# Performance work log

Hardware: AMD Instinct MI355X
Metric: run time of the kernel (lower is better)

Reference implementation:

```python
import jax, jax.numpy as jnp
import numpy as np

EPS = 1e-6
H = 8          # num_heads
GAMMA = 0.99   # fixed decay (requires_grad=False in source)
RPE_LAYERS = 3


def srms(x):
    # SimpleRMSNorm: x / (rms(x) + eps), rms = ||x||_2 / sqrt(d) = sqrt(mean(x^2))
    return x / (jnp.sqrt(jnp.mean(x * x, axis=-1, keepdims=True)) + EPS)


def setup_inputs() -> dict:
    key = jax.random.key(0)
    B, N, E = 8, 2048, 512
    D1 = 1536            # int(3*512) // 8 * 8
    R = 512              # rpe_embedding
    ks = jax.random.split(key, 12)

    def lin(k, i, o):
        return jax.random.normal(k, (i, o), jnp.float32) * (i ** -0.5)

    x = jax.random.normal(ks[0], (B, N, E), jnp.float32)
    return {
        "x": x,
        "Wu": lin(ks[1], E, D1), "bu": jnp.zeros((D1,), jnp.float32),
        "Wv": lin(ks[2], E, D1), "bv": jnp.zeros((D1,), jnp.float32),
        "Wo": lin(ks[3], D1, E), "bo": jnp.zeros((E,), jnp.float32),
        "rpe_Win": lin(ks[4], 1, R), "rpe_bin": jnp.zeros((R,), jnp.float32),
        "rpe_W": jax.random.normal(ks[5], (RPE_LAYERS, R, R), jnp.float32) * (R ** -0.5),
        "rpe_b": jnp.zeros((RPE_LAYERS, R), jnp.float32),
        "rpe_Wout": lin(ks[6], R, D1), "rpe_bout": jnp.zeros((D1,), jnp.float32),
    }


def reference(x, Wu, bu, Wv, bv, Wo, bo, rpe_Win, rpe_bin, rpe_W, rpe_b, rpe_Wout, rpe_bout):
    B, N, E = x.shape
    u = jax.nn.silu(x @ Wu + bu)                     # b n d1
    v = jax.nn.silu(x @ Wv + bv)                     # b n d1
    D1 = v.shape[-1]
    D = D1 // H
    v = v.reshape(B, N, H, D).transpose(0, 2, 1, 3)  # b h n d

    # RPE MLP over positions: row 0 is the zero index, rows 1..N-1 are pos indices 1..N-1 (par_type=1)
    idx = jnp.arange(0, N, dtype=x.dtype)[:, None]   # (N, 1)
    h = idx @ rpe_Win + rpe_bin                      # (N, R)
    for i in range(RPE_LAYERS):                      # residual=False
        h = jax.nn.relu(srms(h)) @ rpe_W[i] + rpe_b[i]
    coeffs = jax.nn.relu(srms(h)) @ rpe_Wout + rpe_bout   # (N, H*D)
    coeffs = coeffs.reshape(N, H, D).transpose(1, 0, 2)   # h n d

    zero = coeffs[:, :1]                             # h 1 d  (a_0)
    pos = coeffs[:, 1:]                              # h n-1 d (a_1..a_{n-1})
    decay = GAMMA ** jnp.arange(1, N, dtype=x.dtype)[None, :, None]
    pos = pos * decay
    # causal: a = [a0, a1..a_{n-1}, a0]; act_type='none' -> identity
    a = jnp.concatenate([zero, pos, zero], axis=1)   # h, n+1, d

    # Toeplitz mixing via circular convolution of length 2n (torch.fft.rfft/irfft, norm='backward')
    m = 2 * N
    yf = jnp.fft.rfft(v, m, axis=2)                  # b h m/2+1 d (complex)
    af = jnp.fft.rfft(a, m, axis=1)[None]            # 1 h m/2+1 d
    out = jnp.fft.irfft(yf * af, m, axis=2)[:, :, :N, :]  # b h n d

    out = out.transpose(0, 2, 1, 3).reshape(B, N, D1)     # b n (h d)
    out = u * out
    return out @ Wo + bo
```

## Files before the change

kernel.cpp:

```cpp
#include <hip/hip_runtime.h>
#include <cstdint>


typedef unsigned short ushort_t;
typedef __attribute__((ext_vector_type(8))) short short8;
typedef __attribute__((ext_vector_type(4))) float f32x4;

#define AS1 __attribute__((address_space(1)))
#define AS3 __attribute__((address_space(3)))

#define SW1(j) ((j) ^ (((j) >> 4) & 15))
#define SW2(j) ((j) ^ ((((j) >> 6) & 7) << 1))

__device__ __forceinline__ float bf2f(ushort_t b) {
  union { unsigned u; float f; } x; x.u = ((unsigned)b) << 16; return x.f;
}
__device__ __forceinline__ ushort_t f2bf(float f) {
  union { float f; unsigned u; } x; x.f = f;
  unsigned r = x.u + 0x7fffu + ((x.u >> 16) & 1u);
  return (ushort_t)(r >> 16);
}

__device__ __forceinline__ void gload_lds16(const void* g, void* l) {
  auto gp = reinterpret_cast<const AS1 unsigned*>(reinterpret_cast<uintptr_t>(g));
  auto lp = reinterpret_cast<AS3 unsigned*>(reinterpret_cast<uintptr_t>(l));
  __builtin_amdgcn_global_load_lds(gp, lp, 16, 0, 0);
}

template<int MODE>
__launch_bounds__(256, 2)
__global__ void gemm_bt(const ushort_t* __restrict__ A, const ushort_t* __restrict__ Bt,
                        const float* __restrict__ bias, void* __restrict__ Cout,
                        void* __restrict__ Cout2, int M, int N, int K, float lng)
{
  __shared__ ushort_t As[128 * 64];
  __shared__ ushort_t Bs[128 * 64];
  const int tid  = threadIdx.x;
  const int wave = tid >> 6, lane = tid & 63;
  const int nb = N >> 7;
  const int bm = (int)blockIdx.x / nb, bn = (int)blockIdx.x % nb;
  const int m0 = bm << 7, n0 = bn << 7;
  const int lrow = lane & 15, quad = lane >> 4;
  const int wm = (wave >> 1) << 6, wn = (wave & 1) << 6;
  const int srow = lane >> 3;
  const int scol = (lane & 7) << 3;

  f32x4 acc[4][4] = {};

  for (int kt = 0; kt < K; kt += 64) {
    __syncthreads();
#pragma unroll
    for (int i = 0; i < 4; ++i) {
      const int ci  = i * 4 + wave;
      const int row = ci * 8 + srow;
      gload_lds16(A  + (long)(m0 + row) * K + kt + scol, (void*)&As[ci * 512]);
      gload_lds16(Bt + (long)(n0 + row) * K + kt + scol, (void*)&Bs[ci * 512]);
    }
    __syncthreads();
#pragma unroll
    for (int s = 0; s < 2; ++s) {
      short8 afr[4], bfr[4];
#pragma unroll
      for (int i = 0; i < 4; ++i)
        afr[i] = *(const short8*)&As[(wm + i * 16 + lrow) * 64 + s * 32 + quad * 8];
#pragma unroll
      for (int j = 0; j < 4; ++j)
        bfr[j] = *(const short8*)&Bs[(wn + j * 16 + lrow) * 64 + s * 32 + quad * 8];
#pragma unroll
      for (int i = 0; i < 4; ++i)
#pragma unroll
        for (int j = 0; j < 4; ++j)
          acc[i][j] = __builtin_amdgcn_mfma_f32_16x16x32_bf16(afr[i], bfr[j], acc[i][j], 0, 0, 0);
    }
  }

#pragma unroll
  for (int i = 0; i < 4; ++i) {
    const int rowb = m0 + wm + i * 16 + quad * 4;
#pragma unroll
    for (int j = 0; j < 4; ++j) {
      const int col = n0 + wn + j * 16 + lrow;
      const float bv = bias[col];
      if (MODE == 0) {
#pragma unroll
        for (int r = 0; r < 4; ++r)
          ((float*)Cout)[(long)(rowb + r) * N + col] = acc[i][j][r] + bv;
      } else if (MODE == 2) {
#pragma unroll
        for (int r = 0; r < 4; ++r) {
          const int row = rowb + r;
          float dec = __expf(lng * (float)row);
          ((float*)Cout)[(long)col * M + row] = (acc[i][j][r] + bv) * dec;
        }
      } else {
        if (col < 1536) {
#pragma unroll
          for (int r = 0; r < 4; ++r) {
            float val = acc[i][j][r] + bv;
            float sv = val / (1.f + __expf(-val));
            ((ushort_t*)Cout)[(long)(rowb + r) * 1536 + col] = f2bf(sv);
          }
        } else {
          union { ushort_t h[4]; uint2 u2; } pk;
#pragma unroll
          for (int r = 0; r < 4; ++r) {
            float val = acc[i][j][r] + bv;
            float sv = val / (1.f + __expf(-val));
            pk.h[r] = f2bf(sv);
          }
          *(uint2*)((ushort_t*)Cout2 + (long)(col - 1536) * 16384 + rowb) = pk.u2;
        }
      }
    }
  }
}

__device__ __forceinline__ void srms_relu_store(float v0, float v1, ushort_t* out,
                                                long rowbase, int tid)
{
  float ss = v0 * v0 + v1 * v1;
#pragma unroll
  for (int off = 32; off; off >>= 1) ss += __shfl_down(ss, off);
  __shared__ float ps[4];
  const int wave = tid >> 6, lane = tid & 63;
  if (lane == 0) ps[wave] = ss;
  __syncthreads();
  float tot = ps[0] + ps[1] + ps[2] + ps[3];
  float sc = 1.f / (sqrtf(tot * (1.f / 512.f)) + 1e-6f);
  out[rowbase + tid]       = f2bf(fmaxf(v0 * sc, 0.f));
  out[rowbase + tid + 256] = f2bf(fmaxf(v1 * sc, 0.f));
}

__launch_bounds__(256)
__global__ void rpe_norm(const float* __restrict__ h, ushort_t* __restrict__ out)
{
  const int n = blockIdx.x, tid = threadIdx.x;
  float v0 = h[(long)n * 512 + tid];
  float v1 = h[(long)n * 512 + tid + 256];
  srms_relu_store(v0, v1, out, (long)n * 512, tid);
}

__device__ __forceinline__ void wtrans_body(const float* __restrict__ src,
                                            ushort_t* __restrict__ dst,
                                            int K, int N, int lb, int tid,
                                            float (*tile)[33])
{
  const int nbx = N >> 5;
  const int bx = lb % nbx, by = lb / nbx;
  const int n0 = bx << 5, k0 = by << 5;
  const int tx = tid & 31, ty = tid >> 5;
  for (int yy = ty; yy < 32; yy += 8)
    tile[yy][tx] = src[(long)(k0 + yy) * N + n0 + tx];
  __syncthreads();
  for (int yy = ty; yy < 32; yy += 8)
    dst[(long)(n0 + yy) * K + k0 + tx] = f2bf(tile[tx][yy]);
}

__launch_bounds__(256)
__global__ void prep_all(const float* __restrict__ Wu, const float* __restrict__ Wv,
                         const float* __restrict__ Wo, const float* __restrict__ rW,
                         const float* __restrict__ rWout,
                         const float* __restrict__ bu, const float* __restrict__ bv,
                         const float* __restrict__ x,
                         const float* __restrict__ rWin, const float* __restrict__ rbin,
                         ushort_t* __restrict__ wuvt, ushort_t* __restrict__ wot,
                         ushort_t* __restrict__ wrt, ushort_t* __restrict__ wroutt,
                         float* __restrict__ buvb, ushort_t* __restrict__ xb,
                         float2* __restrict__ twg, float2* __restrict__ twh,
                         ushort_t* __restrict__ a0)
{
  __shared__ float tile[32][33];
  const int bid = blockIdx.x, tid = threadIdx.x;
  if (bid < 3840) {
    const float* src; ushort_t* dst; int K, N, lb;
    if (bid < 768)       { src = Wu;    dst = wuvt;              K = 512;  N = 1536; lb = bid; }
    else if (bid < 1536) { src = Wv;    dst = wuvt + 1536L*512;  K = 512;  N = 1536; lb = bid - 768; }
    else if (bid < 2304) { src = Wo;    dst = wot;               K = 1536; N = 512;  lb = bid - 1536; }
    else if (bid < 2560) { src = rW;              dst = wrt;              K = 512; N = 512; lb = bid - 2304; }
    else if (bid < 2816) { src = rW + 512L*512;   dst = wrt + 512L*512;   K = 512; N = 512; lb = bid - 2560; }
    else if (bid < 3072) { src = rW + 2L*512*512; dst = wrt + 2L*512*512; K = 512; N = 512; lb = bid - 2816; }
    else                 { src = rWout; dst = wroutt;            K = 512;  N = 1536; lb = bid - 3072; }
    wtrans_body(src, dst, K, N, lb, tid, tile);
  } else if (bid < 3846) {
    int i = (bid - 3840) * 256 + tid;
    if (i < 1536) { buvb[i] = bu[i]; buvb[1536 + i] = bv[i]; }
  } else if (bid < 12038) {
    long i = (long)(bid - 3846) * 1024 + tid * 4;
    float4 f = *(const float4*)(x + i);
    unsigned lo = (unsigned)f2bf(f.x) | ((unsigned)f2bf(f.y) << 16);
    unsigned hi = (unsigned)f2bf(f.z) | ((unsigned)f2bf(f.w) << 16);
    *(uint2*)(xb + i) = make_uint2(lo, hi);
  } else if (bid < 12046) {
    int j = (bid - 12038) * 256 + tid;
    float s, c;
    __sincosf((float)j * (6.283185307179586f / 2048.f), &s, &c);
    twg[j] = make_float2(c, -s);
    if (j <= 1024) {
      float s2, c2;
      __sincosf((float)j * (3.14159265358979f / 2048.f), &s2, &c2);
      twh[j] = make_float2(c2, -s2);
    }
  } else {
    const int n = bid - 12046;
    const float fn = (float)n;
    float v0 = fn * rWin[tid] + rbin[tid];
    float v1 = fn * rWin[tid + 256] + rbin[tid + 256];
    srms_relu_store(v0, v1, a0, (long)n * 512, tid);
  }
}

__device__ __forceinline__ float2 cmulf(float2 a, float2 b) {
  return make_float2(a.x * b.x - a.y * b.y, a.x * b.y + a.y * b.x);
}
__device__ __forceinline__ float2 cadd(float2 a, float2 b){ return make_float2(a.x+b.x, a.y+b.y); }
__device__ __forceinline__ float2 csub(float2 a, float2 b){ return make_float2(a.x-b.x, a.y-b.y); }
__device__ __forceinline__ float2 cmni(float2 z){ return make_float2(z.y, -z.x); }
__device__ __forceinline__ float2 cw8(float2 z){
  const float s = 0.70710678118654752f;
  return make_float2(s*(z.x+z.y), s*(z.y-z.x));
}
__device__ __forceinline__ float2 cw83(float2 z){
  const float s = 0.70710678118654752f;
  return make_float2(s*(z.y-z.x), -s*(z.x+z.y));
}

__device__ __forceinline__ void dft8(const float2* u, float2* y)
{
  float2 a0=cadd(u[0],u[4]), a1=cadd(u[1],u[5]), a2=cadd(u[2],u[6]), a3=cadd(u[3],u[7]);
  float2 b0=csub(u[0],u[4]), b1=cw8(csub(u[1],u[5])), b2=cmni(csub(u[2],u[6])), b3=cw83(csub(u[3],u[7]));
  float2 c0=cadd(a0,a2), c1=csub(a0,a2), c2=cadd(a1,a3), c3=cmni(csub(a1,a3));
  y[0]=cadd(c0,c2); y[2]=cadd(c1,c3); y[4]=csub(c0,c2); y[6]=csub(c1,c3);
  float2 d0=cadd(b0,b2), d1=csub(b0,b2), d2=cadd(b1,b3), d3=cmni(csub(b1,b3));
  y[1]=cadd(d0,d2); y[3]=cadd(d1,d3); y[5]=csub(d0,d2); y[7]=csub(d1,d3);
}
__device__ __forceinline__ void dft8_hz(const float2* u, float2* y)
{
  float2 b1=cw8(u[1]), b2=cmni(u[2]), b3=cw83(u[3]);
  float2 c0=cadd(u[0],u[2]), c1=csub(u[0],u[2]), c2=cadd(u[1],u[3]), c3=cmni(csub(u[1],u[3]));
  y[0]=cadd(c0,c2); y[2]=cadd(c1,c3); y[4]=csub(c0,c2); y[6]=csub(c1,c3);
  float2 d0=cadd(u[0],b2), d1=csub(u[0],b2), d2=cadd(b1,b3), d3=cmni(csub(b1,b3));
  y[1]=cadd(d0,d2); y[3]=cadd(d1,d3); y[5]=csub(d0,d2); y[7]=csub(d1,d3);
}

template<bool HZ>
__device__ void fft2048_r8(float2* b0, float2* b1, const float2* __restrict__ tw, int tid)
{
  float2 u[8], y[8];
  {
    const int i = tid;
#pragma unroll
    for (int m = 0; m < (HZ ? 4 : 8); ++m) u[m] = b0[i + 256 * m];
    if (HZ) dft8_hz(u, y); else dft8(u, y);
    const int j = i << 3;
#pragma unroll
    for (int m = 0; m < 8; ++m) b1[SW1(j + m)] = y[m];
  }
  __syncthreads();
  {
    const int i = tid, k = i & 7, tb = k << 5;
#pragma unroll
    for (int m = 0; m < 8; ++m) u[m] = b1[SW1(i + 256 * m)];
#pragma unroll
    for (int m = 1; m < 8; ++m) u[m] = cmulf(u[m], tw[m * tb]);
    dft8(u, y);
    const int j = ((i - k) << 3) + k;
#pragma unroll
    for (int m = 0; m < 8; ++m) b0[SW2(j + (m << 3))] = y[m];
  }
  __syncthreads();
  {
    const int i = tid, k = i & 63, tb = k << 2;
#pragma unroll
    for (int m = 0; m < 8; ++m) u[m] = b0[SW2(i + 256 * m)];
#pragma unroll
    for (int m = 1; m < 8; ++m) u[m] = cmulf(u[m], tw[m * tb]);
    dft8(u, y);
    const int j = ((i - k) << 3) + k;
#pragma unroll
    for (int m = 0; m < 8; ++m) b1[j + (m << 6)] = y[m];
  }
  __syncthreads();
#pragma unroll
  for (int h = 0; h < 2; ++h) {
    const int i = tid + (h << 8);
    float2 q0 = b1[i], q1 = b1[i + 512], q2 = b1[i + 1024], q3 = b1[i + 1536];
    q1 = cmulf(q1, tw[i]); q2 = cmulf(q2, tw[2 * i]); q3 = cmulf(q3, tw[3 * i]);
    float2 v0 = cadd(q0, q2), v2 = csub(q0, q2);
    float2 v1 = cadd(q1, q3), v3 = cmni(csub(q1, q3));
    b0[i]        = cadd(v0, v1);
    b0[i + 512]  = cadd(v2, v3);
    b0[i + 1024] = csub(v0, v1);
    b0[i + 1536] = csub(v2, v3);
  }
  __syncthreads();
}

__launch_bounds__(256)
__global__ void fft_kernel_spec(const float* __restrict__ kern, float2* __restrict__ af,
                                const float2* __restrict__ twg, const float2* __restrict__ twh)
{
  __shared__ float2 bx[2048], by[2048];
  const int tid = threadIdx.x, c = blockIdx.x;
  const float* kc = kern + (long)c * 2048;
  for (int j = tid; j < 1024; j += 256) bx[j] = *(const float2*)(kc + 2 * j);
  __syncthreads();
  fft2048_r8<true>(bx, by, twg, tid);
  float2* afc = af + (long)c * 2052;
  for (int k = tid; k <= 1024; k += 256) {
    float2 Zk = bx[k], Zn = bx[(2048 - k) & 2047];
    float2 E = make_float2(0.5f * (Zk.x + Zn.x), 0.5f * (Zk.y - Zn.y));
    float2 O = make_float2(0.5f * (Zk.y + Zn.y), 0.5f * (Zn.x - Zk.x));
    float2 W = twh[k];
    float2 WO = cmulf(W, O);
    afc[k] = make_float2(E.x + WO.x, E.y + WO.y);
    if (k != 0 && k != 1024)
      afc[2048 - k] = make_float2(E.x - WO.x, -(E.y - WO.y));
    if (k == 0)
      afc[2048] = make_float2(E.x - WO.x, -(E.y - WO.y));
  }
}

__launch_bounds__(256)
__global__ void fft_conv(ushort_t* __restrict__ vt, const float2* __restrict__ af,
                         const float2* __restrict__ twg, const float2* __restrict__ twh)
{
  __shared__ float2 bx[2048], by[2048];
  const int tid = threadIdx.x;
  const int c = (int)blockIdx.x >> 3;
  ushort_t* vs = vt + (long)blockIdx.x * 2048;
#pragma unroll
  for (int jj = 0; jj < 4; ++jj) {
    const int j = tid + jj * 256;
    unsigned pv = *(const unsigned*)(vs + 2 * j);
    bx[j] = make_float2(bf2f((ushort_t)(pv & 0xffffu)), bf2f((ushort_t)(pv >> 16)));
  }
  __syncthreads();
  fft2048_r8<true>(bx, by, twg, tid);
  const float2* afc = af + (long)c * 2052;
  for (int k = tid; k <= 1024; k += 256) {
    float2 Zk = bx[k], Zn = bx[(2048 - k) & 2047];
    float2 E = make_float2(0.5f * (Zk.x + Zn.x), 0.5f * (Zk.y - Zn.y));
    float2 O = make_float2(0.5f * (Zk.y + Zn.y), 0.5f * (Zn.x - Zk.x));
    float2 W = twh[k];
    float2 WO = cmulf(W, O);
    float2 Xk = make_float2(E.x + WO.x, E.y + WO.y);
    float2 Xn = make_float2(E.x - WO.x, -(E.y - WO.y));
    float2 Pk = cmulf(Xk, afc[k]);
    float2 Pn = cmulf(Xn, afc[2048 - k]);
    float2 E2 = make_float2(0.5f * (Pk.x + Pn.x), 0.5f * (Pk.y - Pn.y));
    float2 G  = make_float2(0.5f * (Pk.x - Pn.x), 0.5f * (Pk.y + Pn.y));
    float2 cW = make_float2(W.x, -W.y);
    float2 Fo = cmulf(cW, G);
    by[k] = make_float2(E2.x - Fo.y, -(E2.y + Fo.x));
    if (k != 0 && k != 1024) {
      const int kn = 2048 - k;
      by[kn] = make_float2(E2.x + Fo.y, E2.y - Fo.x);
    }
  }
  __syncthreads();
  fft2048_r8<false>(by, bx, twg, tid);
  const float inv = 1.f / 2048.f;
#pragma unroll
  for (int jj = 0; jj < 4; ++jj) {
    const int j = tid + jj * 256;
    float2 r = by[j];
    unsigned ov = (unsigned)f2bf(r.x * inv) | ((unsigned)f2bf(-r.y * inv) << 16);
    *(unsigned*)(vs + 2 * j) = ov;
  }
}

__launch_bounds__(256)
__global__ void gate_trans(const ushort_t* __restrict__ convt, ushort_t* __restrict__ u)
{
  __shared__ ushort_t tile[64][65];
  const int bc = (int)blockIdx.x % 24, br = (int)blockIdx.x / 24;
  const int c0 = bc << 6, r0 = br << 6;
  const int tx = threadIdx.x & 63, ty = threadIdx.x >> 6;
  for (int yy = ty; yy < 64; yy += 4)
    tile[yy][tx] = convt[(long)(c0 + yy) * 16384 + r0 + tx];
  __syncthreads();
  for (int yy = ty; yy < 64; yy += 4) {
    long ui = (long)(r0 + yy) * 1536 + c0 + tx;
    float uu = bf2f(u[ui]);
    float cc = bf2f(tile[tx][yy]);
    u[ui] = f2bf(uu * cc);
  }
}

extern "C" void kernel_launch(void* const* d_in, const int* in_sizes, int n_in,
                              void* d_out, int out_size, void* d_ws, size_t ws_size,
                              hipStream_t stream)
{
  const float* x     = (const float*)d_in[0];
  const float* Wu    = (const float*)d_in[1];
  const float* bu    = (const float*)d_in[2];
  const float* Wv    = (const float*)d_in[3];
  const float* bv    = (const float*)d_in[4];
  const float* Wo    = (const float*)d_in[5];
  const float* bo    = (const float*)d_in[6];
  const float* rWin  = (const float*)d_in[7];
  const float* rbin  = (const float*)d_in[8];
  const float* rW    = (const float*)d_in[9];
  const float* rb    = (const float*)d_in[10];
  const float* rWout = (const float*)d_in[11];
  const float* rbout = (const float*)d_in[12];

  char* base = (char*)d_ws;
  size_t off = 0;
  auto alloc = [&](size_t bytes) -> char* {
    size_t r = (off + 255) & ~(size_t)255; off = r + bytes; return base + r;
  };
  ushort_t* wuvt   = (ushort_t*)alloc(3072L * 512 * 2);
  ushort_t* wot    = (ushort_t*)alloc(512L * 1536 * 2);
  ushort_t* wrt    = (ushort_t*)alloc(3L * 512 * 512 * 2);
  ushort_t* wroutt = (ushort_t*)alloc(1536L * 512 * 2);
  float*    buvb   = (float*)   alloc(3072L * 4);
  ushort_t* a0     = (ushort_t*)alloc(2048L * 512 * 2);
  float2*   af     = (float2*)  alloc(1536L * 2052 * 8);
  float2*   twg    = (float2*)  alloc(2048L * 8);
  float2*   twh    = (float2*)  alloc(1025L * 8);
  char*     X      = alloc(16384L * 512 * 2);
  ushort_t* u      = (ushort_t*)alloc(16384L * 1536 * 2);
  ushort_t* vt     = (ushort_t*)alloc(1536L * 16384 * 2);
  ushort_t* xb   = (ushort_t*)X;
  float*    h    = (float*)X;
  float*    kern = (float*)(X + 4L * 1024 * 1024);

  const float lng = -0.01005033585350145f;

  prep_all<<<dim3(14094), dim3(256), 0, stream>>>(
      Wu, Wv, Wo, rW, rWout, bu, bv, x, rWin, rbin,
      wuvt, wot, wrt, wroutt, buvb, xb, twg, twh, a0);

  gemm_bt<3><<<dim3(3072), dim3(256), 0, stream>>>(xb, wuvt, buvb, u, vt,
                                                   16384, 3072, 512, 0.f);

  for (int i = 0; i < 3; ++i) {
    gemm_bt<0><<<dim3(64), dim3(256), 0, stream>>>(a0, wrt + (long)i * 512 * 512,
                                                   rb + (long)i * 512, h, nullptr,
                                                   2048, 512, 512, 0.f);
    rpe_norm<<<dim3(2048), dim3(256), 0, stream>>>(h, a0);
  }
  gemm_bt<2><<<dim3(192), dim3(256), 0, stream>>>(a0, wroutt, rbout, kern, nullptr,
                                                  2048, 1536, 512, lng);
  fft_kernel_spec<<<dim3(1536), dim3(256), 0, stream>>>(kern, af, twg, twh);

  fft_conv<<<dim3(12288), dim3(256), 0, stream>>>(vt, af, twg, twh);
  gate_trans<<<dim3(6144), dim3(256), 0, stream>>>(vt, u);
  gemm_bt<0><<<dim3(512), dim3(256), 0, stream>>>(u, wot, bo, d_out, nullptr,
                                                  16384, 512, 1536, 0.f);
}
```

Before: 511.0 us.

## Run each 2048-point FFT within a single wavefront, in place, without block barriers

Rewrites the 2048-point FFT so one 64-lane wavefront handles a whole row, working in place in a single swizzled LDS buffer. Because each row belongs to one wave, the __syncthreads between stages go away, and each lane now processes 32 points per stage. The FFT kernels launch 128-thread blocks carrying two rows each, which halves LDS use per row. The costs are much higher register pressure (32 complex values per lane) and less parallelism per row. Correctness also depends on the wave executing in lockstep with no explicit LDS barrier.

Result: slower. 559.1 us (+9.4%).

```diff
diff --git a/kernel.cpp b/kernel.cpp
--- a/kernel.cpp
+++ b/kernel.cpp
@@ -8,9 +8,6 @@
 
 #define AS1 __attribute__((address_space(1)))
 #define AS3 __attribute__((address_space(3)))
-
-#define SW1(j) ((j) ^ (((j) >> 4) & 15))
-#define SW2(j) ((j) ^ ((((j) >> 6) & 7) << 1))
 
 __device__ __forceinline__ float bf2f(ushort_t b) {
   union { unsigned u; float f; } x; x.u = ((unsigned)b) << 16; return x.f;
@@ -242,130 +239,187 @@
   y[1]=cadd(d0,d2); y[3]=cadd(d1,d3); y[5]=csub(d0,d2); y[7]=csub(d1,d3);
 }
 
+#define MKBP(B, lam) { (B) + (lam), (B) + ((lam) ^ 4), (B) + ((lam) ^ 8), (B) + ((lam) ^ 12) }
+
 template<bool HZ>
-__device__ void fft2048_r8(float2* b0, float2* b1, const float2* __restrict__ tw, int tid)
-{
-  float2 u[8], y[8];
+__device__ void fft2048_wave(float2* B, const float2* __restrict__ tw, int l)
+{
+  const int lam = l ^ (l >> 4);
+  float2* const Bp[4] = MKBP(B, lam);
+  float2 y[8];
   {
-    const int i = tid;
-#pragma unroll
-    for (int m = 0; m < (HZ ? 4 : 8); ++m) u[m] = b0[i + 256 * m];
-    if (HZ) dft8_hz(u, y); else dft8(u, y);
-    const int j = i << 3;
-#pragma unroll
-    for (int m = 0; m < 8; ++m) b1[SW1(j + m)] = y[m];
-  }
-  __syncthreads();
+    float2 U[4][8];
+#pragma unroll
+    for (int q = 0; q < 4; ++q)
+#pragma unroll
+      for (int m = 0; m < (HZ ? 4 : 8); ++m) {
+        const int t = q + 4 * m;
+        U[q][m] = Bp[t & 3][64 * t];
+      }
+    const int mask1 = (l >> 1) & 15;
+    const int s1base = (l << 3) ^ (mask1 & 8);
+    const int mlow = mask1 & 7;
+#pragma unroll
+    for (int q = 0; q < 4; ++q) {
+      if (HZ) dft8_hz(U[q], y); else dft8(U[q], y);
+#pragma unroll
+      for (int m = 0; m < 8; ++m)
+        B[s1base + 512 * q + (m ^ mlow)] = y[m];
+    }
+  }
   {
-    const int i = tid, k = i & 7, tb = k << 5;
-#pragma unroll
-    for (int m = 0; m < 8; ++m) u[m] = b1[SW1(i + 256 * m)];
-#pragma unroll
-    for (int m = 1; m < 8; ++m) u[m] = cmulf(u[m], tw[m * tb]);
-    dft8(u, y);
-    const int j = ((i - k) << 3) + k;
-#pragma unroll
-    for (int m = 0; m < 8; ++m) b0[SW2(j + (m << 3))] = y[m];
-  }
-  __syncthreads();
+    float2 U[4][8];
+#pragma unroll
+    for (int q = 0; q < 4; ++q)
+#pragma unroll
+      for (int m = 0; m < 8; ++m) {
+        const int t = q + 4 * m;
+        U[q][m] = Bp[t & 3][64 * t];
+      }
+    const int k0 = l & 7;
+    float2 w[8];
+#pragma unroll
+    for (int m = 1; m < 8; ++m) w[m] = tw[32 * k0 * m];
+    const int jb = ((l >> 3) << 6) + k0;
+    const int mask2 = ((l >> 3) & 3) << 2;
+#pragma unroll
+    for (int q = 0; q < 4; ++q) {
+#pragma unroll
+      for (int m = 1; m < 8; ++m) U[q][m] = cmulf(U[q][m], w[m]);
+      dft8(U[q], y);
+#pragma unroll
+      for (int m = 0; m < 8; ++m)
+        B[(jb + 8 * m + 512 * q) ^ (mask2 ^ (m >> 1))] = y[m];
+    }
+  }
   {
-    const int i = tid, k = i & 63, tb = k << 2;
-#pragma unroll
-    for (int m = 0; m < 8; ++m) u[m] = b0[SW2(i + 256 * m)];
-#pragma unroll
-    for (int m = 1; m < 8; ++m) u[m] = cmulf(u[m], tw[m * tb]);
-    dft8(u, y);
-    const int j = ((i - k) << 3) + k;
-#pragma unroll
-    for (int m = 0; m < 8; ++m) b1[j + (m << 6)] = y[m];
-  }
-  __syncthreads();
-#pragma unroll
-  for (int h = 0; h < 2; ++h) {
-    const int i = tid + (h << 8);
-    float2 q0 = b1[i], q1 = b1[i + 512], q2 = b1[i + 1024], q3 = b1[i + 1536];
-    q1 = cmulf(q1, tw[i]); q2 = cmulf(q2, tw[2 * i]); q3 = cmulf(q3, tw[3 * i]);
-    float2 v0 = cadd(q0, q2), v2 = csub(q0, q2);
-    float2 v1 = cadd(q1, q3), v3 = cmni(csub(q1, q3));
-    b0[i]        = cadd(v0, v1);
-    b0[i + 512]  = cadd(v2, v3);
-    b0[i + 1024] = csub(v0, v1);
-    b0[i + 1536] = csub(v2, v3);
-  }
-  __syncthreads();
-}
-
-__launch_bounds__(256)
+    float2 U[4][8];
+#pragma unroll
+    for (int q = 0; q < 4; ++q)
+#pragma unroll
+      for (int m = 0; m < 8; ++m) {
+        const int t = q + 4 * m;
+        U[q][m] = Bp[t & 3][64 * t];
+      }
+    float2 w[8];
+#pragma unroll
+    for (int m = 1; m < 8; ++m) w[m] = tw[4 * l * m];
+#pragma unroll
+    for (int q = 0; q < 4; ++q) {
+#pragma unroll
+      for (int m = 1; m < 8; ++m) U[q][m] = cmulf(U[q][m], w[m]);
+      dft8(U[q], y);
+#pragma unroll
+      for (int m = 0; m < 8; ++m)
+        Bp[m & 3][64 * (m + 8 * q)] = y[m];
+    }
+  }
+#pragma unroll
+  for (int q = 0; q < 8; ++q) {
+    float2 V[4];
+#pragma unroll
+    for (int m = 0; m < 4; ++m)
+      V[m] = Bp[q & 3][64 * (q + 8 * m)];
+    const int i = l + 64 * q;
+    float2 q1 = cmulf(V[1], tw[i]);
+    float2 q2 = cmulf(V[2], tw[2 * i]);
+    float2 q3 = cmulf(V[3], tw[3 * i]);
+    float2 v0 = cadd(V[0], q2), v2 = csub(V[0], q2);
+    float2 v1 = cadd(q1, q3),   v3 = cmni(csub(q1, q3));
+    Bp[q & 3][64 * q]        = cadd(v0, v1);
+    Bp[q & 3][64 * (q + 8)]  = cadd(v2, v3);
+    Bp[q & 3][64 * (q + 16)] = csub(v0, v1);
+    Bp[q & 3][64 * (q + 24)] = csub(v2, v3);
+  }
+}
+
+__launch_bounds__(128)
 __global__ void fft_kernel_spec(const float* __restrict__ kern, float2* __restrict__ af,
                                 const float2* __restrict__ twg, const float2* __restrict__ twh)
 {
-  __shared__ float2 bx[2048], by[2048];
-  const int tid = threadIdx.x, c = blockIdx.x;
+  __shared__ float2 buf[2][2048];
+  const int tid = threadIdx.x, wid = tid >> 6, l = tid & 63;
+  const int c = (int)blockIdx.x * 2 + wid;
+  float2* B = buf[wid];
+  const int lam = l ^ (l >> 4);
+  float2* const Bp[4] = MKBP(B, lam);
   const float* kc = kern + (long)c * 2048;
-  for (int j = tid; j < 1024; j += 256) bx[j] = *(const float2*)(kc + 2 * j);
-  __syncthreads();
-  fft2048_r8<true>(bx, by, twg, tid);
+#pragma unroll
+  for (int t = 0; t < 16; ++t)
+    Bp[t & 3][64 * t] = *(const float2*)(kc + 2 * (l + 64 * t));
+  fft2048_wave<true>(B, twg, l);
   float2* afc = af + (long)c * 2052;
-  for (int k = tid; k <= 1024; k += 256) {
-    float2 Zk = bx[k], Zn = bx[(2048 - k) & 2047];
-    float2 E = make_float2(0.5f * (Zk.x + Zn.x), 0.5f * (Zk.y - Zn.y));
-    float2 O = make_float2(0.5f * (Zk.y + Zn.y), 0.5f * (Zn.x - Zk.x));
-    float2 W = twh[k];
-    float2 WO = cmulf(W, O);
-    afc[k] = make_float2(E.x + WO.x, E.y + WO.y);
-    if (k != 0 && k != 1024)
-      afc[2048 - k] = make_float2(E.x - WO.x, -(E.y - WO.y));
-    if (k == 0)
-      afc[2048] = make_float2(E.x - WO.x, -(E.y - WO.y));
-  }
-}
-
-__launch_bounds__(256)
+#pragma unroll
+  for (int t = 0; t <= 16; ++t) {
+    const int k = l + 64 * t;
+    if (k <= 1024) {
+      float2 Zk = Bp[t & 3][64 * t];
+      const int jn = (2048 - k) & 2047;
+      float2 Zn = B[jn ^ ((jn >> 4) & 15)];
+      float2 E = make_float2(0.5f * (Zk.x + Zn.x), 0.5f * (Zk.y - Zn.y));
+      float2 O = make_float2(0.5f * (Zk.y + Zn.y), 0.5f * (Zn.x - Zk.x));
+      float2 W = twh[k];
+      float2 WO = cmulf(W, O);
+      afc[k] = make_float2(E.x + WO.x, E.y + WO.y);
+      if (k != 0 && k != 1024)
+        afc[2048 - k] = make_float2(E.x - WO.x, -(E.y - WO.y));
+      if (k == 0)
+        afc[2048] = make_float2(E.x - WO.x, -(E.y - WO.y));
+    }
+  }
+}
+
+__launch_bounds__(128)
 __global__ void fft_conv(ushort_t* __restrict__ vt, const float2* __restrict__ af,
                          const float2* __restrict__ twg, const float2* __restrict__ twh)
 {
-  __shared__ float2 bx[2048], by[2048];
-  const int tid = threadIdx.x;
-  const int c = (int)blockIdx.x >> 3;
-  ushort_t* vs = vt + (long)blockIdx.x * 2048;
-#pragma unroll
-  for (int jj = 0; jj < 4; ++jj) {
-    const int j = tid + jj * 256;
-    unsigned pv = *(const unsigned*)(vs + 2 * j);
-    bx[j] = make_float2(bf2f((ushort_t)(pv & 0xffffu)), bf2f((ushort_t)(pv >> 16)));
-  }
-  __syncthreads();
-  fft2048_r8<true>(bx, by, twg, tid);
+  __shared__ float2 buf[2][2048];
+  const int tid = threadIdx.x, wid = tid >> 6, l = tid & 63;
+  const long s = (long)blockIdx.x * 2 + wid;
+  const int c = (int)(s >> 3);
+  float2* B = buf[wid];
+  const int lam = l ^ (l >> 4);
+  float2* const Bp[4] = MKBP(B, lam);
+  ushort_t* vs = vt + s * 2048;
+#pragma unroll
+  for (int t = 0; t < 16; ++t) {
+    unsigned pv = *(const unsigned*)(vs + 2 * (l + 64 * t));
+    Bp[t & 3][64 * t] = make_float2(bf2f((ushort_t)(pv & 0xffffu)), bf2f((ushort_t)(pv >> 16)));
+  }
+  fft2048_wave<true>(B, twg, l);
   const float2* afc = af + (long)c * 2052;
-  for (int k = tid; k <= 1024; k += 256) {
-    float2 Zk = bx[k], Zn = bx[(2048 - k) & 2047];
-    float2 E = make_float2(0.5f * (Zk.x + Zn.x), 0.5f * (Zk.y - Zn.y));
-    float2 O = make_float2(0.5f * (Zk.y + Zn.y), 0.5f * (Zn.x - Zk.x));
-    float2 W = twh[k];
-    float2 WO = cmulf(W, O);
-    float2 Xk = make_float2(E.x + WO.x, E.y + WO.y);
-    float2 Xn = make_float2(E.x - WO.x, -(E.y - WO.y));
-    float2 Pk = cmulf(Xk, afc[k]);
-    float2 Pn = cmulf(Xn, afc[2048 - k]);
-    float2 E2 = make_float2(0.5f * (Pk.x + Pn.x), 0.5f * (Pk.y - Pn.y));
-    float2 G  = make_float2(0.5f * (Pk.x - Pn.x), 0.5f * (Pk.y + Pn.y));
-    float2 cW = make_float2(W.x, -W.y);
-    float2 Fo = cmulf(cW, G);
-    by[k] = make_float2(E2.x - Fo.y, -(E2.y + Fo.x));
-    if (k != 0 && k != 1024) {
-      const int kn = 2048 - k;
-      by[kn] = make_float2(E2.x + Fo.y, E2.y - Fo.x);
-    }
-  }
-  __syncthreads();
-  fft2048_r8<false>(by, bx, twg, tid);
+#pragma unroll
+  for (int t = 0; t <= 16; ++t) {
+    const int k = l + 64 * t;
+    if (k <= 1024) {
+      float2 Zk = Bp[t & 3][64 * t];
+      const int jn = (2048 - k) & 2047;
+      const int sjn = jn ^ ((jn >> 4) & 15);
+      float2 Zn = B[sjn];
+      float2 E = make_float2(0.5f * (Zk.x + Zn.x), 0.5f * (Zk.y - Zn.y));
+      float2 O = make_float2(0.5f * (Zk.y + Zn.y), 0.5f * (Zn.x - Zk.x));
+      float2 W = twh[k];
+      float2 WO = cmulf(W, O);
+      float2 Xk = make_float2(E.x + WO.x, E.y + WO.y);
+      float2 Xn = make_float2(E.x - WO.x, -(E.y - WO.y));
+      float2 Pk = cmulf(Xk, afc[k]);
+      float2 Pn = cmulf(Xn, afc[2048 - k]);
+      float2 E2 = make_float2(0.5f * (Pk.x + Pn.x), 0.5f * (Pk.y - Pn.y));
+      float2 G  = make_float2(0.5f * (Pk.x - Pn.x), 0.5f * (Pk.y + Pn.y));
+      float2 cW = make_float2(W.x, -W.y);
+      float2 Fo = cmulf(cW, G);
+      Bp[t & 3][64 * t] = make_float2(E2.x - Fo.y, -(E2.y + Fo.x));
+      if (k != 0 && k != 1024)
+        B[sjn] = make_float2(E2.x + Fo.y, E2.y - Fo.x);
+    }
+  }
+  fft2048_wave<false>(B, twg, l);
   const float inv = 1.f / 2048.f;
 #pragma unroll
-  for (int jj = 0; jj < 4; ++jj) {
-    const int j = tid + jj * 256;
-    float2 r = by[j];
+  for (int t = 0; t < 16; ++t) {
+    float2 r = Bp[t & 3][64 * t];
     unsigned ov = (unsigned)f2bf(r.x * inv) | ((unsigned)f2bf(-r.y * inv) << 16);
-    *(unsigned*)(vs + 2 * j) = ov;
+    *(unsigned*)(vs + 2 * (l + 64 * t)) = ov;
   }
 }
 
@@ -443,9 +497,9 @@
   }
   gemm_bt<2><<<dim3(192), dim3(256), 0, stream>>>(a0, wroutt, rbout, kern, nullptr,
                                                   2048, 1536, 512, lng);
-  fft_kernel_spec<<<dim3(1536), dim3(256), 0, stream>>>(kern, af, twg, twh);
-
-  fft_conv<<<dim3(12288), dim3(256), 0, stream>>>(vt, af, twg, twh);
+  fft_kernel_spec<<<dim3(768), dim3(128), 0, stream>>>(kern, af, twg, twh);
+
+  fft_conv<<<dim3(6144), dim3(128), 0, stream>>>(vt, af, twg, twh);
   gate_trans<<<dim3(6144), dim3(256), 0, stream>>>(vt, u);
   gemm_bt<0><<<dim3(512), dim3(256), 0, stream>>>(u, wot, bo, d_out, nullptr,
                                                   16384, 512, 1536, 0.f);
```

## Batch two FFT sequences per block and use 64x64 GEMM tiles for small RPE GEMMs

Applied to the files above, without the earlier changes.

The FFT convolution and kernel-spectrum kernels now process two 2048-point sequences per block, sharing twiddle loads and raising per-thread ILP at the cost of 64KB LDS per block. A new 64x64-tile GEMM kernel replaces the 128-tile GEMM for the small RPE MLP and coefficient GEMMs so they launch more blocks and fill the GPU better. The twh table is now fully computed to 2048 entries, with its allocation enlarged to match. Doubling LDS and register use per block may reduce occupancy.

Result: faster. 493.0 us (-3.5%).

```diff
diff --git a/kernel.cpp b/kernel.cpp
--- a/kernel.cpp
+++ b/kernel.cpp
@@ -85,13 +85,6 @@
 #pragma unroll
         for (int r = 0; r < 4; ++r)
           ((float*)Cout)[(long)(rowb + r) * N + col] = acc[i][j][r] + bv;
-      } else if (MODE == 2) {
-#pragma unroll
-        for (int r = 0; r < 4; ++r) {
-          const int row = rowb + r;
-          float dec = __expf(lng * (float)row);
-          ((float*)Cout)[(long)col * M + row] = (acc[i][j][r] + bv) * dec;
-        }
       } else {
         if (col < 1536) {
 #pragma unroll
@@ -110,6 +103,69 @@
           }
           *(uint2*)((ushort_t*)Cout2 + (long)(col - 1536) * 16384 + rowb) = pk.u2;
         }
+      }
+    }
+  }
+}
+
+template<int MODE>
+__launch_bounds__(256, 2)
+__global__ void gemm64_bt(const ushort_t* __restrict__ A, const ushort_t* __restrict__ Bt,
+                          const float* __restrict__ bias, float* __restrict__ Cout,
+                          int M, int N, int K, float lng)
+{
+  __shared__ ushort_t As[64 * 64];
+  __shared__ ushort_t Bs[64 * 64];
+  const int tid = threadIdx.x, wave = tid >> 6, lane = tid & 63;
+  const int nb = N >> 6;
+  const int bm = (int)blockIdx.x / nb, bn = (int)blockIdx.x % nb;
+  const int m0 = bm << 6, n0 = bn << 6;
+  const int lrow = lane & 15, quad = lane >> 4;
+  const int wm = (wave >> 1) << 5, wn = (wave & 1) << 5;
+  const int srow = lane >> 3, scol = (lane & 7) << 3;
+
+  f32x4 acc[2][2] = {};
+
+  for (int kt = 0; kt < K; kt += 64) {
+    __syncthreads();
+#pragma unroll
+    for (int i = 0; i < 2; ++i) {
+      const int ci = i * 4 + wave;
+      const int row = ci * 8 + srow;
+      gload_lds16(A  + (long)(m0 + row) * K + kt + scol, (void*)&As[ci * 512]);
+      gload_lds16(Bt + (long)(n0 + row) * K + kt + scol, (void*)&Bs[ci * 512]);
+    }
+    __syncthreads();
+#pragma unroll
+    for (int s = 0; s < 2; ++s) {
+      short8 afr[2], bfr[2];
+#pragma unroll
+      for (int i = 0; i < 2; ++i)
+        afr[i] = *(const short8*)&As[(wm + i * 16 + lrow) * 64 + s * 32 + quad * 8];
+#pragma unroll
+      for (int j = 0; j < 2; ++j)
+        bfr[j] = *(const short8*)&Bs[(wn + j * 16 + lrow) * 64 + s * 32 + quad * 8];
+#pragma unroll
+      for (int i = 0; i < 2; ++i)
+#pragma unroll
+        for (int j = 0; j < 2; ++j)
+          acc[i][j] = __builtin_amdgcn_mfma_f32_16x16x32_bf16(afr[i], bfr[j], acc[i][j], 0, 0, 0);
+    }
+  }
+
+#pragma unroll
+  for (int i = 0; i < 2; ++i) {
+    const int rowb = m0 + wm + i * 16 + quad * 4;
+#pragma unroll
+    for (int j = 0; j < 2; ++j) {
+      const int col = n0 + wn + j * 16 + lrow;
+      const float bv = bias[col];
+#pragma unroll
+      for (int r = 0; r < 4; ++r) {
+        const int row = rowb + r;
+        float val = acc[i][j][r] + bv;
+        if (MODE == 0) Cout[(long)row * N + col] = val;
+        else           Cout[(long)col * M + row] = val * __expf(lng * (float)row);
       }
     }
   }
@@ -195,11 +251,9 @@
     float s, c;
     __sincosf((float)j * (6.283185307179586f / 2048.f), &s, &c);
     twg[j] = make_float2(c, -s);
-    if (j <= 1024) {
-      float s2, c2;
-      __sincosf((float)j * (3.14159265358979f / 2048.f), &s2, &c2);
-      twh[j] = make_float2(c2, -s2);
-    }
+    float s2, c2;
+    __sincosf((float)j * (3.14159265358979f / 2048.f), &s2, &c2);
+    twh[j] = make_float2(c2, -s2);
   } else {
     const int n = bid - 12046;
     const float fn = (float)n;
@@ -243,129 +297,188 @@
 }
 
 template<bool HZ>
-__device__ void fft2048_r8(float2* b0, float2* b1, const float2* __restrict__ tw, int tid)
-{
-  float2 u[8], y[8];
+__device__ void fft2048_r8_2(float2* b0a, float2* b1a, float2* b0b, float2* b1b,
+                             const float2* __restrict__ tw, int tid)
+{
+  float2 u[8], v[8], y[8], z[8];
   {
     const int i = tid;
 #pragma unroll
-    for (int m = 0; m < (HZ ? 4 : 8); ++m) u[m] = b0[i + 256 * m];
-    if (HZ) dft8_hz(u, y); else dft8(u, y);
+    for (int m = 0; m < (HZ ? 4 : 8); ++m) { u[m] = b0a[i + 256*m]; v[m] = b0b[i + 256*m]; }
+    if (HZ) { dft8_hz(u, y); dft8_hz(v, z); } else { dft8(u, y); dft8(v, z); }
     const int j = i << 3;
 #pragma unroll
-    for (int m = 0; m < 8; ++m) b1[SW1(j + m)] = y[m];
+    for (int m = 0; m < 8; ++m) { b1a[SW1(j + m)] = y[m]; b1b[SW1(j + m)] = z[m]; }
   }
   __syncthreads();
   {
     const int i = tid, k = i & 7, tb = k << 5;
-#pragma unroll
-    for (int m = 0; m < 8; ++m) u[m] = b1[SW1(i + 256 * m)];
-#pragma unroll
-    for (int m = 1; m < 8; ++m) u[m] = cmulf(u[m], tw[m * tb]);
-    dft8(u, y);
+    float2 w[8];
+#pragma unroll
+    for (int m = 1; m < 8; ++m) w[m] = tw[m * tb];
+#pragma unroll
+    for (int m = 0; m < 8; ++m) { u[m] = b1a[SW1(i + 256*m)]; v[m] = b1b[SW1(i + 256*m)]; }
+#pragma unroll
+    for (int m = 1; m < 8; ++m) { u[m] = cmulf(u[m], w[m]); v[m] = cmulf(v[m], w[m]); }
+    dft8(u, y); dft8(v, z);
     const int j = ((i - k) << 3) + k;
 #pragma unroll
-    for (int m = 0; m < 8; ++m) b0[SW2(j + (m << 3))] = y[m];
+    for (int m = 0; m < 8; ++m) { b0a[SW2(j + 8*m)] = y[m]; b0b[SW2(j + 8*m)] = z[m]; }
   }
   __syncthreads();
   {
     const int i = tid, k = i & 63, tb = k << 2;
-#pragma unroll
-    for (int m = 0; m < 8; ++m) u[m] = b0[SW2(i + 256 * m)];
-#pragma unroll
-    for (int m = 1; m < 8; ++m) u[m] = cmulf(u[m], tw[m * tb]);
-    dft8(u, y);
+    float2 w[8];
+#pragma unroll
+    for (int m = 1; m < 8; ++m) w[m] = tw[m * tb];
+#pragma unroll
+    for (int m = 0; m < 8; ++m) { u[m] = b0a[SW2(i + 256*m)]; v[m] = b0b[SW2(i + 256*m)]; }
+#pragma unroll
+    for (int m = 1; m < 8; ++m) { u[m] = cmulf(u[m], w[m]); v[m] = cmulf(v[m], w[m]); }
+    dft8(u, y); dft8(v, z);
     const int j = ((i - k) << 3) + k;
 #pragma unroll
-    for (int m = 0; m < 8; ++m) b1[j + (m << 6)] = y[m];
-  }
-  __syncthreads();
-#pragma unroll
-  for (int h = 0; h < 2; ++h) {
-    const int i = tid + (h << 8);
-    float2 q0 = b1[i], q1 = b1[i + 512], q2 = b1[i + 1024], q3 = b1[i + 1536];
-    q1 = cmulf(q1, tw[i]); q2 = cmulf(q2, tw[2 * i]); q3 = cmulf(q3, tw[3 * i]);
-    float2 v0 = cadd(q0, q2), v2 = csub(q0, q2);
-    float2 v1 = cadd(q1, q3), v3 = cmni(csub(q1, q3));
-    b0[i]        = cadd(v0, v1);
-    b0[i + 512]  = cadd(v2, v3);
-    b0[i + 1024] = csub(v0, v1);
-    b0[i + 1536] = csub(v2, v3);
-  }
-  __syncthreads();
-}
-
-__launch_bounds__(256)
+    for (int m = 0; m < 8; ++m) { b1a[j + 64*m] = y[m]; b1b[j + 64*m] = z[m]; }
+  }
+  __syncthreads();
+#pragma unroll
+  for (int hh = 0; hh < 2; ++hh) {
+    const int i = tid + (hh << 8);
+    float2 w1 = tw[i], w2 = tw[2 * i], w3 = tw[3 * i];
+    float2 q0 = b1a[i], q1 = b1a[i + 512], q2 = b1a[i + 1024], q3 = b1a[i + 1536];
+    float2 r0 = b1b[i], r1 = b1b[i + 512], r2 = b1b[i + 1024], r3 = b1b[i + 1536];
+    q1 = cmulf(q1, w1); q2 = cmulf(q2, w2); q3 = cmulf(q3, w3);
+    r1 = cmulf(r1, w1); r2 = cmulf(r2, w2); r3 = cmulf(r3, w3);
+    {
+      float2 v0 = cadd(q0, q2), v2 = csub(q0, q2);
+      float2 v1 = cadd(q1, q3), v3 = cmni(csub(q1, q3));
+      b0a[i]        = cadd(v0, v1);
+      b0a[i + 512]  = cadd(v2, v3);
+      b0a[i + 1024] = csub(v0, v1);
+      b0a[i + 1536] = csub(v2, v3);
+    }
+    {
+      float2 v0 = cadd(r0, r2), v2 = csub(r0, r2);
+      float2 v1 = cadd(r1, r3), v3 = cmni(csub(r1, r3));
+      b0b[i]        = cadd(v0, v1);
+      b0b[i + 512]  = cadd(v2, v3);
+      b0b[i + 1024] = csub(v0, v1);
+      b0b[i + 1536] = csub(v2, v3);
+    }
+  }
+  __syncthreads();
+}
+
+__launch_bounds__(256, 2)
 __global__ void fft_kernel_spec(const float* __restrict__ kern, float2* __restrict__ af,
                                 const float2* __restrict__ twg, const float2* __restrict__ twh)
 {
-  __shared__ float2 bx[2048], by[2048];
-  const int tid = threadIdx.x, c = blockIdx.x;
-  const float* kc = kern + (long)c * 2048;
-  for (int j = tid; j < 1024; j += 256) bx[j] = *(const float2*)(kc + 2 * j);
-  __syncthreads();
-  fft2048_r8<true>(bx, by, twg, tid);
-  float2* afc = af + (long)c * 2052;
+  __shared__ float2 bx0[2048], by0[2048], bx1[2048], by1[2048];
+  const int tid = threadIdx.x;
+  const int c0 = (int)blockIdx.x * 2;
+  const float* ka = kern + (long)c0 * 2048;
+  const float* kb = ka + 2048;
+  for (int j = tid; j < 1024; j += 256) {
+    bx0[j] = *(const float2*)(ka + 2 * j);
+    bx1[j] = *(const float2*)(kb + 2 * j);
+  }
+  __syncthreads();
+  fft2048_r8_2<true>(bx0, by0, bx1, by1, twg, tid);
+  float2* af0 = af + (long)c0 * 2052;
+  float2* af1 = af0 + 2052;
   for (int k = tid; k <= 1024; k += 256) {
-    float2 Zk = bx[k], Zn = bx[(2048 - k) & 2047];
-    float2 E = make_float2(0.5f * (Zk.x + Zn.x), 0.5f * (Zk.y - Zn.y));
-    float2 O = make_float2(0.5f * (Zk.y + Zn.y), 0.5f * (Zn.x - Zk.x));
-    float2 W = twh[k];
-    float2 WO = cmulf(W, O);
-    afc[k] = make_float2(E.x + WO.x, E.y + WO.y);
-    if (k != 0 && k != 1024)
-      afc[2048 - k] = make_float2(E.x - WO.x, -(E.y - WO.y));
-    if (k == 0)
-      afc[2048] = make_float2(E.x - WO.x, -(E.y - WO.y));
-  }
-}
-
-__launch_bounds__(256)
+    const float2 W = twh[k];
+    const int kn = (2048 - k) & 2047;
+    {
+      float2 Zk = bx0[k], Zn = bx0[kn];
+      float2 E = make_float2(0.5f * (Zk.x + Zn.x), 0.5f * (Zk.y - Zn.y));
+      float2 O = make_float2(0.5f * (Zk.y + Zn.y), 0.5f * (Zn.x - Zk.x));
+      float2 WO = cmulf(W, O);
+      af0[k] = make_float2(E.x + WO.x, E.y + WO.y);
+      if (k != 0 && k != 1024) af0[2048 - k] = make_float2(E.x - WO.x, -(E.y - WO.y));
+      if (k == 0)              af0[2048]     = make_float2(E.x - WO.x, -(E.y - WO.y));
+    }
+    {
+      float2 Zk = bx1[k], Zn = bx1[kn];
+      float2 E = make_float2(0.5f * (Zk.x + Zn.x), 0.5f * (Zk.y - Zn.y));
+      float2 O = make_float2(0.5f * (Zk.y + Zn.y), 0.5f * (Zn.x - Zk.x));
+      float2 WO = cmulf(W, O);
+      af1[k] = make_float2(E.x + WO.x, E.y + WO.y);
+      if (k != 0 && k != 1024) af1[2048 - k] = make_float2(E.x - WO.x, -(E.y - WO.y));
+      if (k == 0)              af1[2048]     = make_float2(E.x - WO.x, -(E.y - WO.y));
+    }
+  }
+}
+
+__launch_bounds__(256, 2)
 __global__ void fft_conv(ushort_t* __restrict__ vt, const float2* __restrict__ af,
                          const float2* __restrict__ twg, const float2* __restrict__ twh)
 {
-  __shared__ float2 bx[2048], by[2048];
+  __shared__ float2 bx0[2048], by0[2048], bx1[2048], by1[2048];
   const int tid = threadIdx.x;
-  const int c = (int)blockIdx.x >> 3;
-  ushort_t* vs = vt + (long)blockIdx.x * 2048;
+  const long s0 = (long)blockIdx.x * 2;
+  const int c = (int)(s0 >> 3);
+  ushort_t* vsa = vt + s0 * 2048;
+  ushort_t* vsb = vsa + 2048;
 #pragma unroll
   for (int jj = 0; jj < 4; ++jj) {
     const int j = tid + jj * 256;
-    unsigned pv = *(const unsigned*)(vs + 2 * j);
-    bx[j] = make_float2(bf2f((ushort_t)(pv & 0xffffu)), bf2f((ushort_t)(pv >> 16)));
-  }
-  __syncthreads();
-  fft2048_r8<true>(bx, by, twg, tid);
+    unsigned pa = *(const unsigned*)(vsa + 2 * j);
+    unsigned pb = *(const unsigned*)(vsb + 2 * j);
+    bx0[j] = make_float2(bf2f((ushort_t)(pa & 0xffffu)), bf2f((ushort_t)(pa >> 16)));
+    bx1[j] = make_float2(bf2f((ushort_t)(pb & 0xffffu)), bf2f((ushort_t)(pb >> 16)));
+  }
+  __syncthreads();
+  fft2048_r8_2<true>(bx0, by0, bx1, by1, twg, tid);
   const float2* afc = af + (long)c * 2052;
   for (int k = tid; k <= 1024; k += 256) {
-    float2 Zk = bx[k], Zn = bx[(2048 - k) & 2047];
-    float2 E = make_float2(0.5f * (Zk.x + Zn.x), 0.5f * (Zk.y - Zn.y));
-    float2 O = make_float2(0.5f * (Zk.y + Zn.y), 0.5f * (Zn.x - Zk.x));
-    float2 W = twh[k];
-    float2 WO = cmulf(W, O);
-    float2 Xk = make_float2(E.x + WO.x, E.y + WO.y);
-    float2 Xn = make_float2(E.x - WO.x, -(E.y - WO.y));
-    float2 Pk = cmulf(Xk, afc[k]);
-    float2 Pn = cmulf(Xn, afc[2048 - k]);
-    float2 E2 = make_float2(0.5f * (Pk.x + Pn.x), 0.5f * (Pk.y - Pn.y));
-    float2 G  = make_float2(0.5f * (Pk.x - Pn.x), 0.5f * (Pk.y + Pn.y));
-    float2 cW = make_float2(W.x, -W.y);
-    float2 Fo = cmulf(cW, G);
-    by[k] = make_float2(E2.x - Fo.y, -(E2.y + Fo.x));
-    if (k != 0 && k != 1024) {
-      const int kn = 2048 - k;
-      by[kn] = make_float2(E2.x + Fo.y, E2.y - Fo.x);
-    }
-  }
-  __syncthreads();
-  fft2048_r8<false>(by, bx, twg, tid);
+    const float2 A0 = afc[k], A1 = afc[2048 - k], W = twh[k];
+    const float2 cW = make_float2(W.x, -W.y);
+    const int kn = (2048 - k) & 2047;
+    {
+      float2 Zk = bx0[k], Zn = bx0[kn];
+      float2 E = make_float2(0.5f * (Zk.x + Zn.x), 0.5f * (Zk.y - Zn.y));
+      float2 O = make_float2(0.5f * (Zk.y + Zn.y), 0.5f * (Zn.x - Zk.x));
+      float2 WO = cmulf(W, O);
+      float2 Xk = make_float2(E.x + WO.x, E.y + WO.y);
+      float2 Xn = make_float2(E.x - WO.x, -(E.y - WO.y));
+      float2 Pk = cmulf(Xk, A0);
+      float2 Pn = cmulf(Xn, A1);
+      float2 E2 = make_float2(0.5f * (Pk.x + Pn.x), 0.5f * (Pk.y - Pn.y));
+      float2 G  = make_float2(0.5f * (Pk.x - Pn.x), 0.5f * (Pk.y + Pn.y));
+      float2 Fo = cmulf(cW, G);
+      by0[k] = make_float2(E2.x - Fo.y, -(E2.y + Fo.x));
+      if (k != 0 && k != 1024)
+        by0[2048 - k] = make_float2(E2.x + Fo.y, E2.y - Fo.x);
+    }
+    {
+      float2 Zk = bx1[k], Zn = bx1[kn];
+      float2 E = make_float2(0.5f * (Zk.x + Zn.x), 0.5f * (Zk.y - Zn.y));
+      float2 O = make_float2(0.5f * (Zk.y + Zn.y), 0.5f * (Zn.x - Zk.x));
+      float2 WO = cmulf(W, O);
+      float2 Xk = make_float2(E.x + WO.x, E.y + WO.y);
+      float2 Xn = make_float2(E.x - WO.x, -(E.y - WO.y));
+      float2 Pk = cmulf(Xk, A0);
+      float2 Pn = cmulf(Xn, A1);
+      float2 E2 = make_float2(0.5f * (Pk.x + Pn.x), 0.5f * (Pk.y - Pn.y));
+      float2 G  = make_float2(0.5f * (Pk.x - Pn.x), 0.5f * (Pk.y + Pn.y));
+      float2 Fo = cmulf(cW, G);
+      by1[k] = make_float2(E2.x - Fo.y, -(E2.y + Fo.x));
+      if (k != 0 && k != 1024)
+        by1[2048 - k] = make_float2(E2.x + Fo.y, E2.y - Fo.x);
+    }
+  }
+  __syncthreads();
+  fft2048_r8_2<false>(by0, bx0, by1, bx1, twg, tid);
   const float inv = 1.f / 2048.f;
 #pragma unroll
   for (int jj = 0; jj < 4; ++jj) {
     const int j = tid + jj * 256;
-    float2 r = by[j];
-    unsigned ov = (unsigned)f2bf(r.x * inv) | ((unsigned)f2bf(-r.y * inv) << 16);
-    *(unsigned*)(vs + 2 * j) = ov;
+    float2 ra = by0[j], rb = by1[j];
+    unsigned oa = (unsigned)f2bf(ra.x * inv) | ((unsigned)f2bf(-ra.y * inv) << 16);
+    unsigned ob = (unsigned)f2bf(rb.x * inv) | ((unsigned)f2bf(-rb.y * inv) << 16);
+    *(unsigned*)(vsa + 2 * j) = oa;
+    *(unsigned*)(vsb + 2 * j) = ob;
   }
 }
 
@@ -418,7 +531,7 @@
   ushort_t* a0     = (ushort_t*)alloc(2048L * 512 * 2);
   float2*   af     = (float2*)  alloc(1536L * 2052 * 8);
   float2*   twg    = (float2*)  alloc(2048L * 8);
-  float2*   twh    = (float2*)  alloc(1025L * 8);
+  float2*   twh    = (float2*)  alloc(2048L * 8);
   char*     X      = alloc(16384L * 512 * 2);
   ushort_t* u      = (ushort_t*)alloc(16384L * 1536 * 2);
   ushort_t* vt     = (ushort_t*)alloc(1536L * 16384 * 2);
@@ -436,16 +549,16 @@
                                                    16384, 3072, 512, 0.f);
 
   for (int i = 0; i < 3; ++i) {
-    gemm_bt<0><<<dim3(64), dim3(256), 0, stream>>>(a0, wrt + (long)i * 512 * 512,
-                                                   rb + (long)i * 512, h, nullptr,
-                                                   2048, 512, 512, 0.f);
+    gemm64_bt<0><<<dim3(256), dim3(256), 0, stream>>>(a0, wrt + (long)i * 512 * 512,
+                                                      rb + (long)i * 512, h,
+                                                      2048, 512, 512, 0.f);
     rpe_norm<<<dim3(2048), dim3(256), 0, stream>>>(h, a0);
   }
-  gemm_bt<2><<<dim3(192), dim3(256), 0, stream>>>(a0, wroutt, rbout, kern, nullptr,
-                                                  2048, 1536, 512, lng);
-  fft_kernel_spec<<<dim3(1536), dim3(256), 0, stream>>>(kern, af, twg, twh);
-
-  fft_conv<<<dim3(12288), dim3(256), 0, stream>>>(vt, af, twg, twh);
+  gemm64_bt<2><<<dim3(768), dim3(256), 0, stream>>>(a0, wroutt, rbout, kern,
+                                                    2048, 1536, 512, lng);
+  fft_kernel_spec<<<dim3(768), dim3(256), 0, stream>>>(kern, af, twg, twh);
+
+  fft_conv<<<dim3(6144), dim3(256), 0, stream>>>(vt, af, twg, twh);
   gate_trans<<<dim3(6144), dim3(256), 0, stream>>>(vt, u);
   gemm_bt<0><<<dim3(512), dim3(256), 0, stream>>>(u, wot, bo, d_out, nullptr,
                                                   16384, 512, 1536, 0.f);
```
